# Kernel optimization log

Measured on AMD Instinct MI355X. Metric: run time of the kernel, lower is better.

The kernel has to match this reference:

```python
import jax, jax.numpy as jnp
import numpy as np

NUM_HEADS = 16
NEG_FILL = -10000.0  # matches torch masked_fill value in source


def setup_inputs() -> dict:
    key = jax.random.key(0)
    ks = jax.random.split(key, 8)
    B, S, H = 4, 2048, 1024
    sc = 1.0 / np.sqrt(H)
    x = jax.random.normal(ks[0], (B, S, H), dtype=jnp.float32)
    L = jax.random.randint(ks[1], (B,), 1, S + 1, dtype=jnp.int64 if jax.config.jax_enable_x64 else jnp.int32)
    Wq = jax.random.normal(ks[2], (H, H), dtype=jnp.float32) * sc
    Wk = jax.random.normal(ks[3], (H, H), dtype=jnp.float32) * sc
    Wv = jax.random.normal(ks[4], (H, H), dtype=jnp.float32) * sc
    bv = jax.random.normal(ks[5], (H,), dtype=jnp.float32) * 0.01
    Wo = jax.random.normal(ks[6], (H, H), dtype=jnp.float32) * sc
    bo = jax.random.normal(ks[7], (H,), dtype=jnp.float32) * 0.01
    return {"x": x, "L": L, "Wq": Wq, "Wk": Wk, "Wv": Wv, "bv": bv, "Wo": Wo, "bo": bo}


def reference(x, L, Wq, Wk, Wv, bv, Wo, bo):
    # AttentionAggregator.forward with L given; dropout in eval mode (identity).
    B, S, H = x.shape
    nh = NUM_HEADS
    dk = H // nh
    # torch nn.Linear: y = x @ W.T + b
    q = (x @ Wq.T).reshape(B, S, nh, dk).transpose(0, 2, 1, 3)  # (B,h,S,dk)
    k = (x @ Wk.T).reshape(B, S, nh, dk).transpose(0, 2, 1, 3)
    v = (x @ Wv.T + bv).reshape(B, S, nh, dk).transpose(0, 2, 1, 3)
    scores = jnp.einsum("bhqd,bhkd->bhqk", q, k) / jnp.sqrt(jnp.float32(dk))
    valid = jnp.arange(S)[None, :] < L[:, None]  # (B,S) True where real token
    scores = jnp.where(valid[:, None, None, :], scores, NEG_FILL)
    attn = jax.nn.softmax(scores, axis=-1)
    ctx = jnp.einsum("bhqk,bhkd->bhqd", attn, v)
    ctx = ctx.transpose(0, 2, 1, 3).reshape(B, S, H)
    attn_out = ctx @ Wo.T + bo  # (B,S,H)
    # masked mean pool over valid positions
    m = valid.astype(x.dtype)  # (B,S)
    pooled = jnp.einsum("bsh,bs->bh", attn_out, m) / m.sum(axis=1, keepdims=True)
    return pooled
```

## Files before the change

kernel.cpp:

```cpp
#include <hip/hip_runtime.h>
#include <hip/hip_bf16.h>
#include <math.h>

constexpr int Bc = 4, Sc = 2048, Hc = 1024, NHc = 16, DKc = 64;

constexpr size_t XHOFF = 0;
constexpr size_t QOFF  = 4194304;
constexpr size_t KOFF  = 8388608;
constexpr size_t WQOFF = 12582912;
constexpr size_t WKOFF = 13107200;
constexpr size_t LIOFF = 13631488;
constexpr size_t WOFF  = 13762560;
constexpr size_t YOFF  = 13893632;
constexpr size_t CSOFF = 13959168;
constexpr size_t YPOFF = 13963264;
constexpr size_t RPOFF = 15011840;
constexpr size_t CPOFF = 15536128;

typedef __attribute__((ext_vector_type(8))) short bf16x8;
typedef __attribute__((ext_vector_type(4))) float f32x4;

__device__ inline short f2bf(float v) {
    __hip_bfloat16 h = __float2bfloat16(v);
    return *reinterpret_cast<short*>(&h);
}

__device__ inline void gld_lds16(const void* g, void* l) {
    __builtin_amdgcn_global_load_lds(
        (const __attribute__((address_space(1))) unsigned int*)g,
        (__attribute__((address_space(3))) unsigned int*)l, 16, 0, 0);
}

__global__ __launch_bounds__(256) void cvt_all_kernel(
    const float* __restrict__ x, const float* __restrict__ Wq,
    const float* __restrict__ Wk, float* __restrict__ ws)
{
    const size_t i = ((size_t)blockIdx.x * 256 + threadIdx.x) * 8;
    const float* src; short* dst; float scale; size_t off;
    if (i < 8388608)       { src = x;  dst = (short*)(ws + XHOFF); off = i;            scale = 1.0f;   }
    else if (i < 9437184)  { src = Wq; dst = (short*)(ws + WQOFF); off = i - 8388608;  scale = 0.125f; }
    else                   { src = Wk; dst = (short*)(ws + WKOFF); off = i - 9437184;  scale = 1.0f;   }
    float4 a = *(const float4*)(src + off);
    float4 b = *(const float4*)(src + off + 4);
    bf16x8 o;
    o[0] = f2bf(a.x * scale); o[1] = f2bf(a.y * scale);
    o[2] = f2bf(a.z * scale); o[3] = f2bf(a.w * scale);
    o[4] = f2bf(b.x * scale); o[5] = f2bf(b.y * scale);
    o[6] = f2bf(b.z * scale); o[7] = f2bf(b.w * scale);
    *(bf16x8*)(dst + off) = o;
}

__global__ __launch_bounds__(256) void proj_mfma_kernel(
    const int* __restrict__ L, float* __restrict__ ws)
{
    const int z  = blockIdx.z;
    const int m0 = blockIdx.y * 128;
    const int n0 = blockIdx.x * 128;
    const int b  = m0 >> 11;
    const int s0 = m0 & 2047;
    const int Lb = L[b];
    if (s0 >= Lb) return;

    const short* __restrict__ A = (const short*)(ws + XHOFF);
    const short* __restrict__ W = (const short*)(ws + (z == 0 ? WQOFF : WKOFF));
    short* __restrict__ Out = (short*)(ws + (z == 0 ? QOFF : KOFF));

    __shared__ __align__(16) short As[128 * 32];
    __shared__ __align__(16) short Bs[128 * 32];

    const int tid  = threadIdx.x;
    const int lane = tid & 63;
    const int wave = tid >> 6;
    const int l16  = lane & 15, quad = lane >> 4;
    const int wm = (wave & 1) * 64, wn = (wave >> 1) * 64;

    const int c0 = tid, c1 = tid + 256;
    const int r0 = c0 >> 2, g0 = (c0 & 3) * 8;
    const int r1 = c1 >> 2, g1 = (c1 & 3) * 8;
    short* lA0 = As + wave * 512;
    short* lA1 = As + 2048 + wave * 512;
    short* lB0 = Bs + wave * 512;
    short* lB1 = Bs + 2048 + wave * 512;

    const f32x4 z4 = {0.f, 0.f, 0.f, 0.f};
    f32x4 acc[4][4];
    #pragma unroll
    for (int i = 0; i < 4; ++i)
        #pragma unroll
        for (int j = 0; j < 4; ++j) acc[i][j] = z4;

    for (int k0 = 0; k0 < Hc; k0 += 32) {
        __syncthreads();
        gld_lds16(A + (size_t)(m0 + r0) * Hc + k0 + g0, lA0);
        gld_lds16(A + (size_t)(m0 + r1) * Hc + k0 + g1, lA1);
        gld_lds16(W + (size_t)(n0 + r0) * Hc + k0 + g0, lB0);
        gld_lds16(W + (size_t)(n0 + r1) * Hc + k0 + g1, lB1);
        __syncthreads();

        bf16x8 af[4], bfr[4];
        #pragma unroll
        for (int mt = 0; mt < 4; ++mt)
            af[mt] = *(const bf16x8*)(As + (wm + mt * 16 + l16) * 32 + quad * 8);
        #pragma unroll
        for (int nt = 0; nt < 4; ++nt)
            bfr[nt] = *(const bf16x8*)(Bs + (wn + nt * 16 + l16) * 32 + quad * 8);
        #pragma unroll
        for (int mt = 0; mt < 4; ++mt)
            #pragma unroll
            for (int nt = 0; nt < 4; ++nt)
                acc[mt][nt] = __builtin_amdgcn_mfma_f32_16x16x32_bf16(
                    af[mt], bfr[nt], acc[mt][nt], 0, 0, 0);
    }

    #pragma unroll
    for (int mt = 0; mt < 4; ++mt) {
        #pragma unroll
        for (int nt = 0; nt < 4; ++nt) {
            const int n = n0 + wn + nt * 16 + l16;
            const int h = n >> 6, d = n & 63;
            #pragma unroll
            for (int r = 0; r < 4; ++r) {
                const int s = s0 + wm + mt * 16 + quad * 4 + r;
                Out[(((size_t)b * NHc + h) * Sc + s) * DKc + d] =
                    f2bf(acc[mt][nt][r]);
            }
        }
    }
}

__global__ __launch_bounds__(256) void rowsum_part_kernel(
    const int* __restrict__ L, float* __restrict__ ws)
{
    const int bh = blockIdx.x;
    const int b  = bh >> 4;
    const int Lb = L[b];
    const int kc0 = blockIdx.z * 512;
    if (blockIdx.y * 128 >= Lb || kc0 >= Lb) return;

    const int tid  = threadIdx.x;
    const int wave = tid >> 6;
    const int lane = tid & 63;
    const int q0 = blockIdx.y * 128 + wave * 32;
    const int l16 = lane & 15, quad = lane >> 4;

    const short* __restrict__ qarr = (const short*)(ws + QOFF) + (size_t)bh * Sc * DKc;
    const short* __restrict__ karr = (const short*)(ws + KOFF) + (size_t)bh * Sc * DKc;

    __shared__ __align__(16) short Ks[128 * 64];

    const short* qrow0 = qarr + (size_t)(q0 + l16) * DKc;
    const short* qrow1 = qarr + (size_t)(q0 + 16 + l16) * DKc;
    const bf16x8 b0lo = *(const bf16x8*)(qrow0 + quad * 8);
    const bf16x8 b0hi = *(const bf16x8*)(qrow0 + 32 + quad * 8);
    const bf16x8 b1lo = *(const bf16x8*)(qrow1 + quad * 8);
    const bf16x8 b1hi = *(const bf16x8*)(qrow1 + 32 + quad * 8);

    const int kend = (kc0 + 512 < Lb) ? kc0 + 512 : Lb;
    float lacc0 = 0.f, lacc1 = 0.f;

    for (int kt = kc0; kt < kend; kt += 128) {
        __syncthreads();
        #pragma unroll
        for (int i = 0; i < 4; ++i) {
            const int s = i * 256 + tid;
            const int row = s >> 3, cc = s & 7, c = cc ^ (row & 7);
            gld_lds16(karr + (size_t)(kt + row) * DKc + c * 8,
                      Ks + (i * 256 + wave * 64) * 8);
        }
        __syncthreads();

        #pragma unroll
        for (int t = 0; t < 8; ++t) {
            const int r = t * 16 + l16;
            const bf16x8 alo = *(const bf16x8*)(Ks + (r * 8 + (quad ^ (r & 7))) * 8);
            const bf16x8 ahi = *(const bf16x8*)(Ks + (r * 8 + ((4 + quad) ^ (r & 7))) * 8);
            f32x4 c0 = {0.f, 0.f, 0.f, 0.f}, c1 = {0.f, 0.f, 0.f, 0.f};
            c0 = __builtin_amdgcn_mfma_f32_16x16x32_bf16(alo, b0lo, c0, 0, 0, 0);
            c0 = __builtin_amdgcn_mfma_f32_16x16x32_bf16(ahi, b0hi, c0, 0, 0, 0);
            c1 = __builtin_amdgcn_mfma_f32_16x16x32_bf16(alo, b1lo, c1, 0, 0, 0);
            c1 = __builtin_amdgcn_mfma_f32_16x16x32_bf16(ahi, b1hi, c1, 0, 0, 0);
            #pragma unroll
            for (int rr = 0; rr < 4; ++rr) {
                const bool kv = (kt + t * 16 + quad * 4 + rr) < kend;
                lacc0 += kv ? __expf(c0[rr]) : 0.f;
                lacc1 += kv ? __expf(c1[rr]) : 0.f;
            }
        }
    }
    lacc0 += __shfl_xor(lacc0, 16, 64); lacc0 += __shfl_xor(lacc0, 32, 64);
    lacc1 += __shfl_xor(lacc1, 16, 64); lacc1 += __shfl_xor(lacc1, 32, 64);
    float* __restrict__ rp = ws + RPOFF + ((size_t)blockIdx.z * 64 + bh) * Sc;
    if (quad == 0) rp[q0 + l16]      = lacc0;
    if (quad == 1) rp[q0 + 16 + l16] = lacc1;
}

__global__ __launch_bounds__(256) void rowsum_reduce_kernel(
    const int* __restrict__ L, float* __restrict__ ws)
{
    const int bh = blockIdx.y;
    const int q  = blockIdx.x * 256 + threadIdx.x;
    const int nc = (L[bh >> 4] + 511) >> 9;
    float acc = 0.f;
    for (int c = 0; c < nc; ++c)
        acc += ws[RPOFF + ((size_t)c * 64 + bh) * Sc + q];
    ws[LIOFF + (size_t)bh * Sc + q] = 1.0f / acc;
}

__global__ __launch_bounds__(256) void colsum_part_kernel(
    const int* __restrict__ L, float* __restrict__ ws)
{
    const int bh = blockIdx.x;
    const int b  = bh >> 4;
    const int Lb = L[b];
    const int qc0 = blockIdx.z * 512;
    if (blockIdx.y * 128 >= Lb || qc0 >= Lb) return;

    const int tid  = threadIdx.x;
    const int wave = tid >> 6;
    const int lane = tid & 63;
    const int k0 = blockIdx.y * 128 + wave * 32;
    const int l16 = lane & 15, quad = lane >> 4;

    const short* __restrict__ qarr = (const short*)(ws + QOFF) + (size_t)bh * Sc * DKc;
    const short* __restrict__ karr = (const short*)(ws + KOFF) + (size_t)bh * Sc * DKc;
    const float* __restrict__ liarr = ws + LIOFF + (size_t)bh * Sc;

    __shared__ __align__(16) short Qs[128 * 64];
    __shared__ __align__(16) float Lis[128];

    const short* krow0 = karr + (size_t)(k0 + l16) * DKc;
    const short* krow1 = karr + (size_t)(k0 + 16 + l16) * DKc;
    const bf16x8 a0lo = *(const bf16x8*)(krow0 + quad * 8);
    const bf16x8 a0hi = *(const bf16x8*)(krow0 + 32 + quad * 8);
    const bf16x8 a1lo = *(const bf16x8*)(krow1 + quad * 8);
    const bf16x8 a1hi = *(const bf16x8*)(krow1 + 32 + quad * 8);

    const int qend = (qc0 + 512 < Lb) ? qc0 + 512 : Lb;
    float w0[4] = {0.f, 0.f, 0.f, 0.f};
    float w1[4] = {0.f, 0.f, 0.f, 0.f};

    for (int qt = qc0; qt < qend; qt += 128) {
        __syncthreads();
        #pragma unroll
        for (int i = 0; i < 4; ++i) {
            const int s = i * 256 + tid;
            const int row = s >> 3, cc = s & 7, c = cc ^ (row & 7);
            gld_lds16(qarr + (size_t)(qt + row) * DKc + c * 8,
                      Qs + (i * 256 + wave * 64) * 8);
        }
        if (tid < 32)
            gld_lds16(liarr + qt + tid * 4, Lis);
        __syncthreads();

        #pragma unroll
        for (int t = 0; t < 8; ++t) {
            const int r = t * 16 + l16;
            const bf16x8 blo = *(const bf16x8*)(Qs + (r * 8 + (quad ^ (r & 7))) * 8);
            const bf16x8 bhi = *(const bf16x8*)(Qs + (r * 8 + ((4 + quad) ^ (r & 7))) * 8);
            const float lv = (qt + r < Lb) ? Lis[r] : 0.f;
            f32x4 c0 = {0.f, 0.f, 0.f, 0.f}, c1 = {0.f, 0.f, 0.f, 0.f};
            c0 = __builtin_amdgcn_mfma_f32_16x16x32_bf16(a0lo, blo, c0, 0, 0, 0);
            c0 = __builtin_amdgcn_mfma_f32_16x16x32_bf16(a0hi, bhi, c0, 0, 0, 0);
            c1 = __builtin_amdgcn_mfma_f32_16x16x32_bf16(a1lo, blo, c1, 0, 0, 0);
            c1 = __builtin_amdgcn_mfma_f32_16x16x32_bf16(a1hi, bhi, c1, 0, 0, 0);
            #pragma unroll
            for (int rr = 0; rr < 4; ++rr) {
                w0[rr] += __expf(c0[rr]) * lv;
                w1[rr] += __expf(c1[rr]) * lv;
            }
        }
    }
    #pragma unroll
    for (int off = 1; off <= 8; off <<= 1) {
        #pragma unroll
        for (int rr = 0; rr < 4; ++rr) {
            w0[rr] += __shfl_xor(w0[rr], off, 64);
            w1[rr] += __shfl_xor(w1[rr], off, 64);
        }
    }
    if (l16 == 0) {
        float* __restrict__ cp = ws + CPOFF + ((size_t)blockIdx.z * 64 + bh) * Sc;
        #pragma unroll
        for (int rr = 0; rr < 4; ++rr) {
            cp[k0 + quad * 4 + rr]      = w0[rr];
            cp[k0 + 16 + quad * 4 + rr] = w1[rr];
        }
    }
}

__global__ __launch_bounds__(256) void colsum_reduce_kernel(
    const int* __restrict__ L, float* __restrict__ ws)
{
    const int bh = blockIdx.y;
    const int k  = blockIdx.x * 256 + threadIdx.x;
    const int nc = (L[bh >> 4] + 511) >> 9;
    float acc = 0.f;
    for (int c = 0; c < nc; ++c)
        acc += ws[CPOFF + ((size_t)c * 64 + bh) * Sc + k];
    ws[WOFF + (size_t)bh * Sc + k] = acc;
}

__global__ __launch_bounds__(256) void yw_part_kernel(
    const float* __restrict__ x, const int* __restrict__ L,
    float* __restrict__ ws)
{
    const int b  = blockIdx.y;
    const int j0 = blockIdx.x * 64;
    const int s0 = blockIdx.z * 128;
    const int Lb = L[b];
    if (s0 >= Lb) return;
    const int js = threadIdx.x & 63;
    const int sl = threadIdx.x >> 6;
    const float* __restrict__ warr = ws + WOFF + (size_t)b * NHc * Sc;
    const float* __restrict__ xb = x + (size_t)b * Sc * Hc;

    __shared__ float wt[128][20];
    __shared__ float red[4][16][64];

    #pragma unroll
    for (int i = 0; i < 8; ++i) {
        const int s = (threadIdx.x & 15) + 16 * i;
        const int h = threadIdx.x >> 4;
        float v = 0.f;
        if (s0 + s < Lb) v = warr[(size_t)h * Sc + s0 + s];
        wt[s][h] = v;
    }
    __syncthreads();

    float acc[16];
    #pragma unroll
    for (int h = 0; h < 16; ++h) acc[h] = 0.f;

    #pragma unroll 4
    for (int s = sl; s < 128; s += 4) {
        const float xv = xb[(size_t)(s0 + s) * Hc + j0 + js];
        const f32x4 wa = *(const f32x4*)&wt[s][0];
        const f32x4 wb = *(const f32x4*)&wt[s][4];
        const f32x4 wc = *(const f32x4*)&wt[s][8];
        const f32x4 wd = *(const f32x4*)&wt[s][12];
        #pragma unroll
        for (int h = 0; h < 4; ++h) acc[h]      += wa[h] * xv;
        #pragma unroll
        for (int h = 0; h < 4; ++h) acc[4 + h]  += wb[h] * xv;
        #pragma unroll
        for (int h = 0; h < 4; ++h) acc[8 + h]  += wc[h] * xv;
        #pragma unroll
        for (int h = 0; h < 4; ++h) acc[12 + h] += wd[h] * xv;
    }
    #pragma unroll
    for (int h = 0; h < 16; ++h) red[sl][h][js] = acc[h];
    __syncthreads();
    if (sl == 0) {
        float* __restrict__ yp = ws + YPOFF +
            ((size_t)blockIdx.z * Bc * NHc + (size_t)b * NHc) * Hc;
        #pragma unroll
        for (int h = 0; h < 16; ++h)
            yp[(size_t)h * Hc + j0 + js] =
                red[0][h][js] + red[1][h][js] + red[2][h][js] + red[3][h][js];
    }
}

__global__ __launch_bounds__(256) void yw_reduce_kernel(
    const int* __restrict__ L, float* __restrict__ ws)
{
    const int b = blockIdx.y;
    const int i = blockIdx.x * 256 + threadIdx.x;
    const int nc = (L[b] + 127) >> 7;
    const float* __restrict__ p = ws + YPOFF + (size_t)b * NHc * Hc + i;
    float acc = 0.f;
    for (int c = 0; c < nc; ++c)
        acc += p[(size_t)c * Bc * NHc * Hc];
    ws[YOFF + (size_t)b * NHc * Hc + i] = acc;
}

__global__ __launch_bounds__(256) void csum_kernel(
    const float* __restrict__ Wv, const float* __restrict__ bv,
    const int* __restrict__ L, float* __restrict__ ws)
{
    const int b = blockIdx.y;
    const int h = blockIdx.x;
    const int n0 = h * 64;
    const int lane = threadIdx.x & 63;
    const int wave = threadIdx.x >> 6;
    const float Lb = (float)L[b];

    __shared__ float ys[1024];
    const float* __restrict__ y = ws + YOFF + ((size_t)b * NHc + h) * Hc;
    for (int i = threadIdx.x; i < 1024; i += 256) ys[i] = y[i];
    __syncthreads();

    f32x4 yv[4];
    #pragma unroll
    for (int p = 0; p < 4; ++p) yv[p] = *(const f32x4*)&ys[p * 256 + lane * 4];

    #pragma unroll
    for (int r = 0; r < 16; ++r) {
        const int n = n0 + wave * 16 + r;
        const float* wrow = Wv + (size_t)n * Hc;
        float a = 0.f;
        #pragma unroll
        for (int p = 0; p < 4; ++p) {
            const f32x4 wv = *(const f32x4*)(wrow + p * 256 + lane * 4);
            a += wv[0]*yv[p][0] + wv[1]*yv[p][1] + wv[2]*yv[p][2] + wv[3]*yv[p][3];
        }
        #pragma unroll
        for (int off = 32; off > 0; off >>= 1) a += __shfl_xor(a, off, 64);
        if (lane == 0)
            ws[CSOFF + (size_t)b * Hc + n] = a + bv[n] * Lb;
    }
}

__global__ __launch_bounds__(256) void out_kernel(
    const float* __restrict__ Wo, const float* __restrict__ bo,
    const int* __restrict__ L, const float* __restrict__ ws,
    float* __restrict__ out)
{
    const int b = blockIdx.y;
    const int o0 = blockIdx.x * 64;
    const int lane = threadIdx.x & 63;
    const int wave = threadIdx.x >> 6;
    const float linv = 1.0f / (float)L[b];

    __shared__ float cs[1024];
    const float* __restrict__ c = ws + CSOFF + (size_t)b * Hc;
    for (int i = threadIdx.x; i < 1024; i += 256) cs[i] = c[i];
    __syncthreads();

    f32x4 cv[4];
    #pragma unroll
    for (int p = 0; p < 4; ++p) cv[p] = *(const f32x4*)&cs[p * 256 + lane * 4];

    #pragma unroll
    for (int r = 0; r < 16; ++r) {
        const int o = o0 + wave * 16 + r;
        const float* wrow = Wo + (size_t)o * Hc;
        float a = 0.f;
        #pragma unroll
        for (int p = 0; p < 4; ++p) {
            const f32x4 wv = *(const f32x4*)(wrow + p * 256 + lane * 4);
            a += wv[0]*cv[p][0] + wv[1]*cv[p][1] + wv[2]*cv[p][2] + wv[3]*cv[p][3];
        }
        #pragma unroll
        for (int off = 32; off > 0; off >>= 1) a += __shfl_xor(a, off, 64);
        if (lane == 0)
            out[(size_t)b * Hc + o] = a * linv + bo[o];
    }
}

extern "C" void kernel_launch(void* const* d_in, const int* in_sizes, int n_in,
                              void* d_out, int out_size, void* d_ws, size_t ws_size,
                              hipStream_t stream)
{
    (void)in_sizes; (void)n_in; (void)out_size; (void)ws_size;
    const float* x  = (const float*)d_in[0];
    const int*   L  = (const int*)d_in[1];
    const float* Wq = (const float*)d_in[2];
    const float* Wk = (const float*)d_in[3];
    const float* Wv = (const float*)d_in[4];
    const float* bv = (const float*)d_in[5];
    const float* Wo = (const float*)d_in[6];
    const float* bo = (const float*)d_in[7];
    float* out = (float*)d_out;
    float* ws  = (float*)d_ws;

    cvt_all_kernel<<<5120, 256, 0, stream>>>(x, Wq, Wk, ws);

    dim3 gp(Hc / 128, (Bc * Sc) / 128, 2);
    proj_mfma_kernel<<<gp, 256, 0, stream>>>(L, ws);

    dim3 gr(Bc * NHc, Sc / 128, 4);
    rowsum_part_kernel<<<gr, 256, 0, stream>>>(L, ws);
    dim3 grr(Sc / 256, Bc * NHc);
    rowsum_reduce_kernel<<<grr, 256, 0, stream>>>(L, ws);

    dim3 gcp(Bc * NHc, Sc / 128, 4);
    colsum_part_kernel<<<gcp, 256, 0, stream>>>(L, ws);
    colsum_reduce_kernel<<<grr, 256, 0, stream>>>(L, ws);

    dim3 gy(Hc / 64, Bc, Sc / 128);
    yw_part_kernel<<<gy, 256, 0, stream>>>(x, L, ws);

    dim3 gyr((NHc * Hc) / 256, Bc);
    yw_reduce_kernel<<<gyr, 256, 0, stream>>>(L, ws);

    dim3 gc(NHc, Bc);
    csum_kernel<<<gc, 256, 0, stream>>>(Wv, bv, L, ws);

    dim3 go(Hc / 64, Bc);
    out_kernel<<<go, 256, 0, stream>>>(Wo, bo, L, ws, out);
}
```

Before: 243.6 us.

## Split attention row/col sums into 128-key chunks and use exp2 with folded log2e

The key/query chunk per block in the rowsum and colsum kernels shrinks from 512 to 128, so the grid's z-dimension grows to 16 and each block loads one tile with no loop. A branch that skips masking is added for fully valid tiles. The Q scale now folds in log2(e), so the raw hardware exp2 instruction can replace __expf. The partial buffers are moved to overlap the YP region, which relies on those regions not being live at the same time. The reduce kernels now sum more partials, which adds reduction traffic.

```diff
diff --git a/kernel.cpp b/kernel.cpp
--- a/kernel.cpp
+++ b/kernel.cpp
@@ -14,8 +14,8 @@
 constexpr size_t YOFF  = 13893632;
 constexpr size_t CSOFF = 13959168;
 constexpr size_t YPOFF = 13963264;
-constexpr size_t RPOFF = 15011840;
-constexpr size_t CPOFF = 15536128;
+constexpr size_t RPOFF = 13963264;
+constexpr size_t CPOFF = 13963264;
 
 typedef __attribute__((ext_vector_type(8))) short bf16x8;
 typedef __attribute__((ext_vector_type(4))) float f32x4;
@@ -23,6 +23,14 @@
 __device__ inline short f2bf(float v) {
     __hip_bfloat16 h = __float2bfloat16(v);
     return *reinterpret_cast<short*>(&h);
+}
+
+__device__ inline float ex2(float x) {
+#if defined(__has_builtin) && __has_builtin(__builtin_amdgcn_exp2f)
+    return __builtin_amdgcn_exp2f(x);
+#else
+    float r; asm("v_exp_f32 %0, %1" : "=v"(r) : "v"(x)); return r;
+#endif
 }
 
 __device__ inline void gld_lds16(const void* g, void* l) {
@@ -37,9 +45,10 @@
 {
     const size_t i = ((size_t)blockIdx.x * 256 + threadIdx.x) * 8;
     const float* src; short* dst; float scale; size_t off;
-    if (i < 8388608)       { src = x;  dst = (short*)(ws + XHOFF); off = i;            scale = 1.0f;   }
-    else if (i < 9437184)  { src = Wq; dst = (short*)(ws + WQOFF); off = i - 8388608;  scale = 0.125f; }
-    else                   { src = Wk; dst = (short*)(ws + WKOFF); off = i - 9437184;  scale = 1.0f;   }
+    constexpr float QSC = 0.125f * 1.44269504088896340736f;
+    if (i < 8388608)       { src = x;  dst = (short*)(ws + XHOFF); off = i;            scale = 1.0f; }
+    else if (i < 9437184)  { src = Wq; dst = (short*)(ws + WQOFF); off = i - 8388608;  scale = QSC;  }
+    else                   { src = Wk; dst = (short*)(ws + WKOFF); off = i - 9437184;  scale = 1.0f; }
     float4 a = *(const float4*)(src + off);
     float4 b = *(const float4*)(src + off + 4);
     bf16x8 o;
@@ -134,7 +143,7 @@
     const int bh = blockIdx.x;
     const int b  = bh >> 4;
     const int Lb = L[b];
-    const int kc0 = blockIdx.z * 512;
+    const int kc0 = blockIdx.z * 128;
     if (blockIdx.y * 128 >= Lb || kc0 >= Lb) return;
 
     const int tid  = threadIdx.x;
@@ -155,20 +164,33 @@
     const bf16x8 b1lo = *(const bf16x8*)(qrow1 + quad * 8);
     const bf16x8 b1hi = *(const bf16x8*)(qrow1 + 32 + quad * 8);
 
-    const int kend = (kc0 + 512 < Lb) ? kc0 + 512 : Lb;
+    #pragma unroll
+    for (int i = 0; i < 4; ++i) {
+        const int s = i * 256 + tid;
+        const int row = s >> 3, cc = s & 7, c = cc ^ (row & 7);
+        gld_lds16(karr + (size_t)(kc0 + row) * DKc + c * 8,
+                  Ks + (i * 256 + wave * 64) * 8);
+    }
+    __syncthreads();
+
     float lacc0 = 0.f, lacc1 = 0.f;
-
-    for (int kt = kc0; kt < kend; kt += 128) {
-        __syncthreads();
-        #pragma unroll
-        for (int i = 0; i < 4; ++i) {
-            const int s = i * 256 + tid;
-            const int row = s >> 3, cc = s & 7, c = cc ^ (row & 7);
-            gld_lds16(karr + (size_t)(kt + row) * DKc + c * 8,
-                      Ks + (i * 256 + wave * 64) * 8);
-        }
-        __syncthreads();
-
+    if (kc0 + 128 <= Lb) {
+        #pragma unroll
+        for (int t = 0; t < 8; ++t) {
+            const int r = t * 16 + l16;
+            const bf16x8 alo = *(const bf16x8*)(Ks + (r * 8 + (quad ^ (r & 7))) * 8);
+            const bf16x8 ahi = *(const bf16x8*)(Ks + (r * 8 + ((4 + quad) ^ (r & 7))) * 8);
+            f32x4 c0 = {0.f, 0.f, 0.f, 0.f}, c1 = {0.f, 0.f, 0.f, 0.f};
+            c0 = __builtin_amdgcn_mfma_f32_16x16x32_bf16(alo, b0lo, c0, 0, 0, 0);
+            c0 = __builtin_amdgcn_mfma_f32_16x16x32_bf16(ahi, b0hi, c0, 0, 0, 0);
+            c1 = __builtin_amdgcn_mfma_f32_16x16x32_bf16(alo, b1lo, c1, 0, 0, 0);
+            c1 = __builtin_amdgcn_mfma_f32_16x16x32_bf16(ahi, b1hi, c1, 0, 0, 0);
+            const float e0 = ex2(c0[0]), e1 = ex2(c0[1]), e2 = ex2(c0[2]), e3 = ex2(c0[3]);
+            const float f0 = ex2(c1[0]), f1 = ex2(c1[1]), f2 = ex2(c1[2]), f3 = ex2(c1[3]);
+            lacc0 += (e0 + e1) + (e2 + e3);
+            lacc1 += (f0 + f1) + (f2 + f3);
+        }
+    } else {
         #pragma unroll
         for (int t = 0; t < 8; ++t) {
             const int r = t * 16 + l16;
@@ -181,9 +203,9 @@
             c1 = __builtin_amdgcn_mfma_f32_16x16x32_bf16(ahi, b1hi, c1, 0, 0, 0);
             #pragma unroll
             for (int rr = 0; rr < 4; ++rr) {
-                const bool kv = (kt + t * 16 + quad * 4 + rr) < kend;
-                lacc0 += kv ? __expf(c0[rr]) : 0.f;
-                lacc1 += kv ? __expf(c1[rr]) : 0.f;
+                const bool kv = (kc0 + t * 16 + quad * 4 + rr) < Lb;
+                lacc0 += kv ? ex2(c0[rr]) : 0.f;
+                lacc1 += kv ? ex2(c1[rr]) : 0.f;
             }
         }
     }
@@ -199,7 +221,7 @@
 {
     const int bh = blockIdx.y;
     const int q  = blockIdx.x * 256 + threadIdx.x;
-    const int nc = (L[bh >> 4] + 511) >> 9;
+    const int nc = (L[bh >> 4] + 127) >> 7;
     float acc = 0.f;
     for (int c = 0; c < nc; ++c)
         acc += ws[RPOFF + ((size_t)c * 64 + bh) * Sc + q];
@@ -212,7 +234,7 @@
     const int bh = blockIdx.x;
     const int b  = bh >> 4;
     const int Lb = L[b];
-    const int qc0 = blockIdx.z * 512;
+    const int qc0 = blockIdx.z * 128;
     if (blockIdx.y * 128 >= Lb || qc0 >= Lb) return;
 
     const int tid  = threadIdx.x;
@@ -235,29 +257,27 @@
     const bf16x8 a1lo = *(const bf16x8*)(krow1 + quad * 8);
     const bf16x8 a1hi = *(const bf16x8*)(krow1 + 32 + quad * 8);
 
-    const int qend = (qc0 + 512 < Lb) ? qc0 + 512 : Lb;
+    #pragma unroll
+    for (int i = 0; i < 4; ++i) {
+        const int s = i * 256 + tid;
+        const int row = s >> 3, cc = s & 7, c = cc ^ (row & 7);
+        gld_lds16(qarr + (size_t)(qc0 + row) * DKc + c * 8,
+                  Qs + (i * 256 + wave * 64) * 8);
+    }
+    if (tid < 32)
+        gld_lds16(liarr + qc0 + tid * 4, Lis);
+    __syncthreads();
+
     float w0[4] = {0.f, 0.f, 0.f, 0.f};
     float w1[4] = {0.f, 0.f, 0.f, 0.f};
 
-    for (int qt = qc0; qt < qend; qt += 128) {
-        __syncthreads();
-        #pragma unroll
-        for (int i = 0; i < 4; ++i) {
-            const int s = i * 256 + tid;
-            const int row = s >> 3, cc = s & 7, c = cc ^ (row & 7);
-            gld_lds16(qarr + (size_t)(qt + row) * DKc + c * 8,
-                      Qs + (i * 256 + wave * 64) * 8);
-        }
-        if (tid < 32)
-            gld_lds16(liarr + qt + tid * 4, Lis);
-        __syncthreads();
-
+    if (qc0 + 128 <= Lb) {
         #pragma unroll
         for (int t = 0; t < 8; ++t) {
             const int r = t * 16 + l16;
             const bf16x8 blo = *(const bf16x8*)(Qs + (r * 8 + (quad ^ (r & 7))) * 8);
             const bf16x8 bhi = *(const bf16x8*)(Qs + (r * 8 + ((4 + quad) ^ (r & 7))) * 8);
-            const float lv = (qt + r < Lb) ? Lis[r] : 0.f;
+            const float lv = Lis[r];
             f32x4 c0 = {0.f, 0.f, 0.f, 0.f}, c1 = {0.f, 0.f, 0.f, 0.f};
             c0 = __builtin_amdgcn_mfma_f32_16x16x32_bf16(a0lo, blo, c0, 0, 0, 0);
             c0 = __builtin_amdgcn_mfma_f32_16x16x32_bf16(a0hi, bhi, c0, 0, 0, 0);
@@ -265,8 +285,26 @@
             c1 = __builtin_amdgcn_mfma_f32_16x16x32_bf16(a1hi, bhi, c1, 0, 0, 0);
             #pragma unroll
             for (int rr = 0; rr < 4; ++rr) {
-                w0[rr] += __expf(c0[rr]) * lv;
-                w1[rr] += __expf(c1[rr]) * lv;
+                w0[rr] += ex2(c0[rr]) * lv;
+                w1[rr] += ex2(c1[rr]) * lv;
+            }
+        }
+    } else {
+        #pragma unroll
+        for (int t = 0; t < 8; ++t) {
+            const int r = t * 16 + l16;
+            const bf16x8 blo = *(const bf16x8*)(Qs + (r * 8 + (quad ^ (r & 7))) * 8);
+            const bf16x8 bhi = *(const bf16x8*)(Qs + (r * 8 + ((4 + quad) ^ (r & 7))) * 8);
+            const float lv = (qc0 + r < Lb) ? Lis[r] : 0.f;
+            f32x4 c0 = {0.f, 0.f, 0.f, 0.f}, c1 = {0.f, 0.f, 0.f, 0.f};
+            c0 = __builtin_amdgcn_mfma_f32_16x16x32_bf16(a0lo, blo, c0, 0, 0, 0);
+            c0 = __builtin_amdgcn_mfma_f32_16x16x32_bf16(a0hi, bhi, c0, 0, 0, 0);
+            c1 = __builtin_amdgcn_mfma_f32_16x16x32_bf16(a1lo, blo, c1, 0, 0, 0);
+            c1 = __builtin_amdgcn_mfma_f32_16x16x32_bf16(a1hi, bhi, c1, 0, 0, 0);
+            #pragma unroll
+            for (int rr = 0; rr < 4; ++rr) {
+                w0[rr] += ex2(c0[rr]) * lv;
+                w1[rr] += ex2(c1[rr]) * lv;
             }
         }
     }
@@ -293,7 +331,7 @@
 {
     const int bh = blockIdx.y;
     const int k  = blockIdx.x * 256 + threadIdx.x;
-    const int nc = (L[bh >> 4] + 511) >> 9;
+    const int nc = (L[bh >> 4] + 127) >> 7;
     float acc = 0.f;
     for (int c = 0; c < nc; ++c)
         acc += ws[CPOFF + ((size_t)c * 64 + bh) * Sc + k];
@@ -468,12 +506,12 @@
     dim3 gp(Hc / 128, (Bc * Sc) / 128, 2);
     proj_mfma_kernel<<<gp, 256, 0, stream>>>(L, ws);
 
-    dim3 gr(Bc * NHc, Sc / 128, 4);
+    dim3 gr(Bc * NHc, Sc / 128, 16);
     rowsum_part_kernel<<<gr, 256, 0, stream>>>(L, ws);
     dim3 grr(Sc / 256, Bc * NHc);
     rowsum_reduce_kernel<<<grr, 256, 0, stream>>>(L, ws);
 
-    dim3 gcp(Bc * NHc, Sc / 128, 4);
+    dim3 gcp(Bc * NHc, Sc / 128, 16);
     colsum_part_kernel<<<gcp, 256, 0, stream>>>(L, ws);
     colsum_reduce_kernel<<<grr, 256, 0, stream>>>(L, ws);
 
```

Result: no change. 240.9 us (-1.1%).
